# Performance work log

Measured on AMD Instinct MI355X. Metric: run time of the kernel, lower is better.

The kernel has to match this reference:

```python
import jax, jax.numpy as jnp
import numpy as np

D_IN = 1024
D_OUT = 1024
NUM_HEADS = 16
HEAD_DIM = D_OUT // NUM_HEADS


def setup_inputs() -> dict:
    key = jax.random.key(0)
    ks = jax.random.split(key, 6)
    s = 1.0 / np.sqrt(D_IN)
    inputs = jax.random.normal(ks[0], (4, 2048, D_IN), dtype=jnp.float32)
    Wq = jax.random.uniform(ks[1], (D_IN, D_OUT), jnp.float32, -s, s)
    Wk = jax.random.uniform(ks[2], (D_IN, D_OUT), jnp.float32, -s, s)
    Wv = jax.random.uniform(ks[3], (D_IN, D_OUT), jnp.float32, -s, s)
    so = 1.0 / np.sqrt(D_OUT)
    Wo = jax.random.uniform(ks[4], (D_OUT, D_OUT), jnp.float32, -so, so)
    bo = jax.random.uniform(ks[5], (D_OUT,), jnp.float32, -so, so)
    return {"inputs": inputs, "Wq": Wq, "Wk": Wk, "Wv": Wv, "Wo": Wo, "bo": bo}


def reference(inputs, Wq, Wk, Wv, Wo, bo):
    b, n, _ = inputs.shape
    # projections -> [b, h, n, d]
    def split_heads(x):
        return x.reshape(b, n, NUM_HEADS, HEAD_DIM).transpose(0, 2, 1, 3)
    q = split_heads(inputs @ Wq)
    k = split_heads(inputs @ Wk)
    v = split_heads(inputs @ Wv)
    scores = jnp.einsum('bhqd,bhkd->bhqk', q, k) / np.sqrt(HEAD_DIM).astype(np.float32)
    causal = jnp.tril(jnp.ones((n, n), dtype=bool))  # True = keep
    scores = jnp.where(causal, scores, -jnp.inf)
    weights = jax.nn.softmax(scores, axis=-1)
    ctx = jnp.einsum('bhqk,bhkd->bhqd', weights, v)
    ctx = ctx.transpose(0, 2, 1, 3).reshape(b, n, D_OUT)
    return ctx @ Wo + bo
```

## Files before the change

### kernel.cpp

```cpp
#include <hip/hip_runtime.h>

typedef unsigned short u16;
typedef unsigned int u32;
typedef __attribute__((ext_vector_type(8))) short short8;
typedef __attribute__((ext_vector_type(4))) short short4_t;
typedef __attribute__((ext_vector_type(4))) float floatx4;
typedef __attribute__((ext_vector_type(4))) unsigned short ushort4_t;
typedef __attribute__((ext_vector_type(4))) float float4_t;
typedef __attribute__((ext_vector_type(2))) unsigned int uint2_t;


__device__ __forceinline__ u16 f2bf(float f) {
  unsigned u = __builtin_bit_cast(unsigned, f);
  u += 0x7FFFu + ((u >> 16) & 1u);
  return (u16)(u >> 16);
}

__device__ __forceinline__ u32 cvt_pk_bf16(float a, float b) {
  u32 r;
  asm("v_cvt_pk_bf16_f32 %0, %1, %2" : "=v"(r) : "v"(a), "v"(b));
  return r;
}

__device__ __forceinline__ void gload_lds16(const void* g, void* l) {
  __builtin_amdgcn_global_load_lds(
      (const __attribute__((address_space(1))) void*)g,
      (__attribute__((address_space(3))) void*)l, 16, 0, 0);
}

#define BAR __builtin_amdgcn_s_barrier()
#define LGK0                                              \
  do {                                                    \
    asm volatile("s_waitcnt lgkmcnt(0)" ::: "memory");    \
    __builtin_amdgcn_sched_barrier(0);                    \
  } while (0)
#define VM4 asm volatile("s_waitcnt vmcnt(4)" ::: "memory")
#define VM0 asm volatile("s_waitcnt vmcnt(0)" ::: "memory")

__device__ __forceinline__ int vscr(int d, int c6) {
  int kp = (c6 >> 2) ^ (2 * (d & 7)) ^ ((d >> 3) & 1);
  return kp * 4 + (c6 & 3);
}


__global__ void cvt_x(const float* __restrict__ src, u16* __restrict__ dst) {
  int i = blockIdx.x * 256 + threadIdx.x;
  float4_t f = ((const float4_t*)src)[i];
  ushort4_t u;
  u.x = f2bf(f.x); u.y = f2bf(f.y); u.z = f2bf(f.z); u.w = f2bf(f.w);
  ((ushort4_t*)dst)[i] = u;
}

__global__ __launch_bounds__(256) void transpose_cvt4(
    const float* __restrict__ wq, const float* __restrict__ wk,
    const float* __restrict__ wv, const float* __restrict__ wo,
    u16* __restrict__ qk, u16* __restrict__ vt, u16* __restrict__ ot, float sc) {
  __shared__ float T[64][65];
  const int which = blockIdx.z;
  const float* s = (which == 0) ? wq : (which == 1) ? wk : (which == 2) ? wv : wo;
  u16* d = (which == 0) ? qk : (which == 1) ? (qk + (1u << 20)) : (which == 2) ? vt : ot;
  const float scale = (which == 0) ? sc : 1.f;
  const int n0 = blockIdx.x * 64, k0 = blockIdx.y * 64;
  const int c = threadIdx.x & 63, rg = threadIdx.x >> 6;
  for (int i = 0; i < 16; ++i) {
    int r = i * 4 + rg;
    T[r][c] = s[(k0 + r) * 1024 + n0 + c];
  }
  __syncthreads();
  for (int i = 0; i < 16; ++i) {
    int r = i * 4 + rg;
    d[(n0 + r) * 1024 + k0 + c] = f2bf(T[c][r] * scale);
  }
}

template <int MODE>
__global__ __launch_bounds__(256) void gemm_bt(
    const u16* __restrict__ A, const u16* __restrict__ Bt, void* __restrict__ Cv,
    const float* __restrict__ bias, int K, int lda, int ldb, int ldc) {
  __shared__ u16 As[2][128 * 32];
  __shared__ u16 Bs[2][128 * 32];
  const int tid = threadIdx.x;
  const int w = tid >> 6, l = tid & 63, quad = l >> 4, l16 = l & 15;
  const int wm = w >> 1, wn = w & 1;
  const size_t m0 = (size_t)blockIdx.y * 128, n0 = (size_t)blockIdx.x * 128;

  floatx4 acc[4][4];
  for (int i = 0; i < 4; ++i)
    for (int j = 0; j < 4; ++j) acc[i][j] = (floatx4){0.f, 0.f, 0.f, 0.f};

  auto stage = [&](int k0, int buf) {
    for (int i = 0; i < 2; ++i) {
      int c = i * 256 + tid;
      int row = c >> 2, off = (c & 3) * 8;
      gload_lds16(A + (m0 + row) * (size_t)lda + k0 + off, &As[buf][c * 8]);
      gload_lds16(Bt + (n0 + row) * (size_t)ldb + k0 + off, &Bs[buf][c * 8]);
    }
  };

  const int nk = K >> 5;
  stage(0, 0);
  __syncthreads();

  for (int ki = 0; ki < nk; ++ki) {
    const int buf = ki & 1;
    if (ki + 1 < nk) stage((ki + 1) << 5, buf ^ 1);

    short8 a[4], bb[4];
    for (int im = 0; im < 4; ++im)
      a[im] = *(const short8*)&As[buf][(wm * 64 + im * 16 + l16) * 32 + quad * 8];
    for (int in = 0; in < 4; ++in)
      bb[in] = *(const short8*)&Bs[buf][(wn * 64 + in * 16 + l16) * 32 + quad * 8];
    for (int im = 0; im < 4; ++im)
      for (int in = 0; in < 4; ++in)
        acc[im][in] = __builtin_amdgcn_mfma_f32_16x16x32_bf16(a[im], bb[in], acc[im][in], 0, 0, 0);

    __syncthreads();
  }

  for (int im = 0; im < 4; ++im)
    for (int in = 0; in < 4; ++in) {
      size_t r0 = m0 + wm * 64 + im * 16 + quad * 4;
      size_t col = n0 + wn * 64 + in * 16 + l16;
      float bv = (MODE == 1) ? bias[col] : 0.f;
      for (int r = 0; r < 4; ++r) {
        float val = acc[im][in][r] + bv;
        if (MODE == 0) {
          ((u16*)Cv)[(r0 + r) * (size_t)ldc + col] = f2bf(val);
        } else if (MODE == 1) {
          ((float*)Cv)[(r0 + r) * (size_t)ldc + col] = val;
        } else {
          int row = (int)(r0 + r);
          size_t ncol = (col & ~(size_t)63) | (size_t)vscr(row, (int)(col & 63));
          ((u16*)Cv)[row * (size_t)ldc + ncol] = f2bf(val);
        }
      }
    }
}

__global__ __launch_bounds__(512, 2) void gemm256_bt(
    const u16* __restrict__ A, const u16* __restrict__ Bt, u16* __restrict__ C,
    int K, int lda, int ldb, int ldc) {
  __shared__ u16 As[2][256 * 64];
  __shared__ u16 Bs[2][256 * 64];
  const int tid = threadIdx.x;
  const int l = tid & 63, quad = l >> 4, l16 = l & 15;
  const int w = tid >> 6, wm = w >> 2, wn = w & 3;

  const int orig = blockIdx.x + 8 * blockIdx.y;
  const int tsw = (orig & 7) * 32 + (orig >> 3);
  const size_t m0 = (size_t)(tsw >> 3) * 256, n0 = (size_t)(tsw & 7) * 256;
  const int NT = K >> 6;

  floatx4 acc[8][4];
#pragma unroll
  for (int i = 0; i < 8; ++i)
#pragma unroll
    for (int j = 0; j < 4; ++j) acc[i][j] = (floatx4){0.f, 0.f, 0.f, 0.f};

  auto stage = [&](int isB, int t, int h) {
    const u16* src = isB ? Bt : A;
    const size_t rb = isB ? n0 : m0;
    const int ld = isB ? ldb : lda;
    u16* lds = (isB ? &Bs[t & 1][0] : &As[t & 1][0]) + h * 8192;
    const int k0 = t << 6;
#pragma unroll
    for (int r = 0; r < 2; ++r) {
      int idx = r * 512 + tid;
      int rr = idx >> 3;
      int ce = ((idx & 7) ^ (rr & 7)) << 3;
      gload_lds16(src + (rb + h * 128 + rr) * (size_t)ld + k0 + ce, lds + idx * 8);
    }
  };

  const int swz = (l16 & 7) << 4;
  const int ca0 = (quad * 16) ^ swz;
  const int ca1 = (64 + quad * 16) ^ swz;
  const char* aB = (const char*)&As[0][0];
  const char* bB = (const char*)&Bs[0][0];
  const int arow = (wm * 128 + l16) * 128;
  const int brow = (wn * 64 + l16) * 128;

  short8 a[4][2], b[2][2][2];

  auto readA = [&](int buf, int mh) {
#pragma unroll
    for (int ii = 0; ii < 4; ++ii) {
      const char* p = aB + buf * 32768 + arow + mh * 8192 + ii * 2048;
      a[ii][0] = *(const short8*)(p + ca0);
      a[ii][1] = *(const short8*)(p + ca1);
    }
  };
  auto readB = [&](int buf, int nh) {
#pragma unroll
    for (int jj = 0; jj < 2; ++jj) {
      const char* p = bB + buf * 32768 + brow + nh * 4096 + jj * 2048;
      b[nh][jj][0] = *(const short8*)(p + ca0);
      b[nh][jj][1] = *(const short8*)(p + ca1);
    }
  };
  auto mmaq = [&](int mh, int nh) {
    __builtin_amdgcn_s_setprio(1);
#pragma unroll
    for (int ii = 0; ii < 4; ++ii)
#pragma unroll
      for (int jj = 0; jj < 2; ++jj) {
        acc[mh * 4 + ii][nh * 2 + jj] = __builtin_amdgcn_mfma_f32_16x16x32_bf16(
            a[ii][0], b[nh][jj][0], acc[mh * 4 + ii][nh * 2 + jj], 0, 0, 0);
        acc[mh * 4 + ii][nh * 2 + jj] = __builtin_amdgcn_mfma_f32_16x16x32_bf16(
            a[ii][1], b[nh][jj][1], acc[mh * 4 + ii][nh * 2 + jj], 0, 0, 0);
      }
    __builtin_amdgcn_s_setprio(0);
  };

  stage(1, 0, 0); stage(1, 0, 1); stage(0, 0, 0); stage(0, 0, 1);
  stage(1, 1, 0); stage(1, 1, 1);
  VM4;
  BAR;

  const int nit = NT >> 1;
  for (int i = 0; i < nit; ++i) {
    const int t0 = 2 * i;
    const bool last = (i + 1 == nit);
    readA(0, 0); readB(0, 0);
    stage(0, t0 + 1, 0);
    BAR; LGK0; mmaq(0, 0); BAR;
    readB(0, 1);
    stage(0, t0 + 1, 1);
    BAR; LGK0; mmaq(0, 1); BAR;
    readA(0, 1);
    if (t0 + 2 < NT) stage(1, t0 + 2, 0);
    BAR; LGK0; mmaq(1, 1); BAR;
    if (t0 + 2 < NT) stage(1, t0 + 2, 1);
    mmaq(1, 0);
    if (last) { VM0; } else { VM4; }
    BAR;
    readA(1, 0); readB(1, 0);
    if (t0 + 2 < NT) stage(0, t0 + 2, 0);
    BAR; LGK0; mmaq(0, 0); BAR;
    readB(1, 1);
    if (t0 + 2 < NT) stage(0, t0 + 2, 1);
    BAR; LGK0; mmaq(0, 1); BAR;
    readA(1, 1);
    if (t0 + 3 < NT) stage(1, t0 + 3, 0);
    BAR; LGK0; mmaq(1, 1); BAR;
    if (t0 + 3 < NT) stage(1, t0 + 3, 1);
    mmaq(1, 0);
    VM4; BAR;
  }

#pragma unroll
  for (int iF = 0; iF < 8; ++iF)
#pragma unroll
    for (int jF = 0; jF < 4; ++jF) {
      size_t r0 = m0 + wm * 128 + iF * 16 + quad * 4;
      size_t col = n0 + wn * 64 + jF * 16 + l16;
#pragma unroll
      for (int r = 0; r < 4; ++r)
        C[(r0 + r) * (size_t)ldc + col] = f2bf(acc[iF][jF][r]);
    }
}

__global__ __launch_bounds__(512, 4) void flash_attn(
    const u16* __restrict__ QK, const u16* __restrict__ Vt, u16* __restrict__ ctx) {
  __shared__ u16 Ks[2][64 * 64];
  __shared__ u16 Vs[2][64 * 64];

  const int tid = threadIdx.x;
  const int w = tid >> 6, l = tid & 63, quad = l >> 4, l16 = l & 15;
  const int bh = blockIdx.x, p = blockIdx.y;
  const int b = bh >> 4, h = bh & 15;
  const int xr = (l16 & 7) << 4;
  const int xv = (2 * (l16 & 7)) ^ ((l16 >> 3) & 1);

  const int qtA = 15 - p, qtB = p;
  const int nktA = 2 * qtA + 2, ntot = nktA + 2 * qtB + 2;

  auto stage = [&](int kt, int buf) {
    int c = tid;
    int row = c >> 3;
    int scolK = ((c & 7) ^ (row & 7)) << 3;
    gload_lds16(QK + (size_t)(b * 2048 + kt * 64 + row) * 2048 + 1024 + h * 64 + scolK,
                &Ks[buf][c * 8]);
    gload_lds16(Vt + (size_t)(h * 64 + row) * 8192 + b * 2048 + kt * 64 + ((c & 7) << 3),
                &Vs[buf][c * 8]);
  };

  short8 aq[2];
  floatx4 o[4];
  float lsum;

  auto load_q = [&](int q0w) {
    const size_t base = (size_t)(b * 2048 + q0w + l16) * 2048 + h * 64 + quad * 8;
    aq[0] = *(const short8*)(QK + base);
    aq[1] = *(const short8*)(QK + base + 32);
    lsum = 0.f;
    for (int df = 0; df < 4; ++df) o[df] = (floatx4){0.f, 0.f, 0.f, 0.f};
  };

  auto epilogue = [&](int q0w) {
    float t = lsum;
    t += __shfl_xor(t, 16, 64);
    t += __shfl_xor(t, 32, 64);
    float inv = __builtin_amdgcn_rcpf(t);
    size_t row = (size_t)(b * 2048 + q0w + l16);
    for (int df = 0; df < 4; ++df) {
      ushort4_t st;
      for (int r = 0; r < 4; ++r) st[r] = f2bf(o[df][r] * inv);
      *(ushort4_t*)(ctx + row * 1024 + h * 64 + df * 16 + quad * 4) = st;
    }
  };

  int q0w = qtA * 128 + w * 16;
  int ktmax_w = (q0w + 15) >> 6;
  load_q(q0w);
  stage(0, 0);
  __syncthreads();

  for (int t = 0; t < ntot; ++t) {
    const int buf = t & 1;
    const int kt = (t < nktA) ? t : t - nktA;
    if (t + 1 < ntot) {
      int tn = t + 1;
      stage((tn < nktA) ? tn : tn - nktA, buf ^ 1);
    }

    if (kt <= ktmax_w) {
      const bool need_mask = (kt == ktmax_w);

      short8 ka[4][2];
      for (int nf = 0; nf < 4; ++nf) {
        const char* kb = (const char*)&Ks[buf][0] + (nf * 16 + l16) * 128;
        ka[nf][0] = *(const short8*)(kb + ((quad * 16) ^ xr));
        ka[nf][1] = *(const short8*)(kb + ((64 + quad * 16) ^ xr));
      }

      floatx4 s[4];
      for (int nf = 0; nf < 4; ++nf) s[nf] = (floatx4){0.f, 0.f, 0.f, 0.f};
      __builtin_amdgcn_s_setprio(1);
      for (int nf = 0; nf < 4; ++nf) {
        s[nf] = __builtin_amdgcn_mfma_f32_16x16x32_bf16(ka[nf][0], aq[0], s[nf], 0, 0, 0);
        s[nf] = __builtin_amdgcn_mfma_f32_16x16x32_bf16(ka[nf][1], aq[1], s[nf], 0, 0, 0);
      }
      __builtin_amdgcn_s_setprio(0);
      if (need_mask) {
        int qpos = q0w + l16;
        for (int nf = 0; nf < 4; ++nf)
          for (int r = 0; r < 4; ++r) {
            int kpos = kt * 64 + nf * 16 + quad * 4 + r;
            if (kpos > qpos) s[nf][r] = -1e30f;
          }
      }
      for (int nf = 0; nf < 4; ++nf) {
        const int kpp = ((nf * 4 + quad) ^ xv) << 3;
        short4_t va[4];
        for (int df = 0; df < 4; ++df) {
          const char* vb = (const char*)&Vs[buf][0] + (df * 16 + l16) * 128;
          va[df] = *(const short4_t*)(vb + kpp);
        }
        float p0 = __builtin_amdgcn_exp2f(s[nf][0]);
        float p1 = __builtin_amdgcn_exp2f(s[nf][1]);
        float p2 = __builtin_amdgcn_exp2f(s[nf][2]);
        float p3 = __builtin_amdgcn_exp2f(s[nf][3]);
        lsum += (p0 + p1) + (p2 + p3);
        uint2_t pk;
        pk.x = cvt_pk_bf16(p0, p1);
        pk.y = cvt_pk_bf16(p2, p3);
        short4_t pb = __builtin_bit_cast(short4_t, pk);
        __builtin_amdgcn_s_setprio(1);
        for (int df = 0; df < 4; ++df)
          o[df] = __builtin_amdgcn_mfma_f32_16x16x16bf16_1k(va[df], pb, o[df], 0, 0, 0);
        __builtin_amdgcn_s_setprio(0);
      }
    }
    __syncthreads();

    if (t == nktA - 1) {
      epilogue(q0w);
      q0w = qtB * 128 + w * 16;
      ktmax_w = (q0w + 15) >> 6;
      load_q(q0w);
    }
  }
  epilogue(q0w);
}


extern "C" void kernel_launch(void* const* d_in, const int* in_sizes, int n_in,
                              void* d_out, int out_size, void* d_ws, size_t ws_size,
                              hipStream_t stream) {
  const float* X  = (const float*)d_in[0];
  const float* Wq = (const float*)d_in[1];
  const float* Wk = (const float*)d_in[2];
  const float* Wv = (const float*)d_in[3];
  const float* Wo = (const float*)d_in[4];
  const float* bo = (const float*)d_in[5];

  char* ws = (char*)d_ws;
  u16* Xb   = (u16*)(ws);
  u16* WqkT = (u16*)(ws + (16u << 20));
  u16* WvT  = (u16*)(ws + (20u << 20));
  u16* WoT  = (u16*)(ws + (22u << 20));
  u16* QKb  = (u16*)(ws + (24u << 20));
  u16* Vt   = (u16*)(ws + (56u << 20));

  const float SC = 0.125f * 1.44269504088896340736f;

  cvt_x<<<8192, 256, 0, stream>>>(X, Xb);
  transpose_cvt4<<<dim3(16, 16, 4), 256, 0, stream>>>(Wq, Wk, Wv, Wo, WqkT, WvT, WoT, SC);

  gemm256_bt<<<dim3(8, 32), 512, 0, stream>>>(Xb, WqkT, QKb, 1024, 1024, 1024, 2048);
  gemm_bt<2><<<dim3(64, 8), 256, 0, stream>>>(WvT, Xb, Vt, nullptr, 1024, 1024, 1024, 8192);

  flash_attn<<<dim3(64, 8), 512, 0, stream>>>(QKb, Vt, Xb);

  gemm_bt<1><<<dim3(8, 64), 256, 0, stream>>>(Xb, WoT, (float*)d_out, bo, 1024, 1024, 1024, 1024);
}
```

Baseline: 242.4 us.

## Launch one q-tile per attention block instead of pairing heavy and light tiles

The flash attention kernel no longer pairs a long causal q-tile with a short one inside a single block. Each block now handles one 128-row q-tile, and the grid doubles to 16 tiles in y. This removes the mid-loop epilogue and Q reload, and it exposes more blocks for occupancy. The cost is that per-block work becomes very uneven, so balancing now depends on the hardware scheduler.

```diff
diff --git a/kernel.cpp b/kernel.cpp
--- a/kernel.cpp
+++ b/kernel.cpp
@@ -267,13 +267,13 @@
 
   const int tid = threadIdx.x;
   const int w = tid >> 6, l = tid & 63, quad = l >> 4, l16 = l & 15;
-  const int bh = blockIdx.x, p = blockIdx.y;
+  const int bh = blockIdx.x;
+  const int qt = 15 - blockIdx.y;
   const int b = bh >> 4, h = bh & 15;
   const int xr = (l16 & 7) << 4;
   const int xv = (2 * (l16 & 7)) ^ ((l16 >> 3) & 1);
 
-  const int qtA = 15 - p, qtB = p;
-  const int nktA = 2 * qtA + 2, ntot = nktA + 2 * qtB + 2;
+  const int nkt = 2 * qt + 2;
 
   auto stage = [&](int kt, int buf) {
     int c = tid;
@@ -285,44 +285,26 @@
                 &Vs[buf][c * 8]);
   };
 
+  const int q0w = qt * 128 + w * 16;
+  const int ktmax_w = (q0w + 15) >> 6;
+
   short8 aq[2];
   floatx4 o[4];
   float lsum;
-
-  auto load_q = [&](int q0w) {
+  {
     const size_t base = (size_t)(b * 2048 + q0w + l16) * 2048 + h * 64 + quad * 8;
     aq[0] = *(const short8*)(QK + base);
     aq[1] = *(const short8*)(QK + base + 32);
     lsum = 0.f;
     for (int df = 0; df < 4; ++df) o[df] = (floatx4){0.f, 0.f, 0.f, 0.f};
-  };
-
-  auto epilogue = [&](int q0w) {
-    float t = lsum;
-    t += __shfl_xor(t, 16, 64);
-    t += __shfl_xor(t, 32, 64);
-    float inv = __builtin_amdgcn_rcpf(t);
-    size_t row = (size_t)(b * 2048 + q0w + l16);
-    for (int df = 0; df < 4; ++df) {
-      ushort4_t st;
-      for (int r = 0; r < 4; ++r) st[r] = f2bf(o[df][r] * inv);
-      *(ushort4_t*)(ctx + row * 1024 + h * 64 + df * 16 + quad * 4) = st;
-    }
-  };
-
-  int q0w = qtA * 128 + w * 16;
-  int ktmax_w = (q0w + 15) >> 6;
-  load_q(q0w);
+  }
+
   stage(0, 0);
   __syncthreads();
 
-  for (int t = 0; t < ntot; ++t) {
-    const int buf = t & 1;
-    const int kt = (t < nktA) ? t : t - nktA;
-    if (t + 1 < ntot) {
-      int tn = t + 1;
-      stage((tn < nktA) ? tn : tn - nktA, buf ^ 1);
-    }
+  for (int kt = 0; kt < nkt; ++kt) {
+    const int buf = kt & 1;
+    if (kt + 1 < nkt) stage(kt + 1, buf ^ 1);
 
     if (kt <= ktmax_w) {
       const bool need_mask = (kt == ktmax_w);
@@ -373,15 +355,20 @@
       }
     }
     __syncthreads();
-
-    if (t == nktA - 1) {
-      epilogue(q0w);
-      q0w = qtB * 128 + w * 16;
-      ktmax_w = (q0w + 15) >> 6;
-      load_q(q0w);
-    }
-  }
-  epilogue(q0w);
+  }
+
+  {
+    float t = lsum;
+    t += __shfl_xor(t, 16, 64);
+    t += __shfl_xor(t, 32, 64);
+    float inv = __builtin_amdgcn_rcpf(t);
+    size_t row = (size_t)(b * 2048 + q0w + l16);
+    for (int df = 0; df < 4; ++df) {
+      ushort4_t st;
+      for (int r = 0; r < 4; ++r) st[r] = f2bf(o[df][r] * inv);
+      *(ushort4_t*)(ctx + row * 1024 + h * 64 + df * 16 + quad * 4) = st;
+    }
+  }
 }
 
 
@@ -411,7 +398,7 @@
   gemm256_bt<<<dim3(8, 32), 512, 0, stream>>>(Xb, WqkT, QKb, 1024, 1024, 1024, 2048);
   gemm_bt<2><<<dim3(64, 8), 256, 0, stream>>>(WvT, Xb, Vt, nullptr, 1024, 1024, 1024, 8192);
 
-  flash_attn<<<dim3(64, 8), 512, 0, stream>>>(QKb, Vt, Xb);
+  flash_attn<<<dim3(64, 16), 512, 0, stream>>>(QKb, Vt, Xb);
 
   gemm_bt<1><<<dim3(8, 64), 256, 0, stream>>>(Xb, WoT, (float*)d_out, bo, 1024, 1024, 1024, 1024);
 }
```

Measured after the change: 244.9 us, median of 2. About the same (+1.0%).
